# Optimization experiments

Hardware: AMD Instinct MI355X
Metric: run time of the kernel (lower is better)

## Reference

```python
import jax, jax.numpy as jnp
import numpy as np

B, N, D, H = 4, 1024, 1024, 16
DH = D // H
NEG_BIG = -2.0**32 + 1.0  # padding value from the torch code


def setup_inputs() -> dict:
    key = jax.random.key(0)
    ks = jax.random.split(key, 12)
    inp = {
        "x": jax.random.normal(ks[0], (B, N, D), dtype=jnp.float32),
        "key_padding_mask": jnp.zeros((B, N), dtype=bool),  # True = padded
        # attention projections (nn.Linear, bias=False): y = x @ W.T
        "Wq": jax.random.normal(ks[1], (D, D), dtype=jnp.float32) * (D ** -0.5),
        "Wk": jax.random.normal(ks[2], (D, D), dtype=jnp.float32) * (D ** -0.5),
        "Wv": jax.random.normal(ks[3], (D, D), dtype=jnp.float32) * (D ** -0.5),
        # FFN
        "W1": jax.random.normal(ks[4], (D, D), dtype=jnp.float32) * (D ** -0.5),
        "b1": jnp.zeros((D,), dtype=jnp.float32),
        "W2": jax.random.normal(ks[5], (D, D), dtype=jnp.float32) * (D ** -0.5),
        "b2": jnp.zeros((D,), dtype=jnp.float32),
        # MaskedLayerNorm params
        "g1": jnp.ones((D,), dtype=jnp.float32),
        "beta1": jnp.zeros((D,), dtype=jnp.float32),
        "g2": jnp.ones((D,), dtype=jnp.float32),
        "beta2": jnp.zeros((D,), dtype=jnp.float32),
    }
    return inp


def masked_layer_norm(x, scale, bias, eps=1e-5):
    mean = jnp.mean(x, axis=-1, keepdims=True)
    var = jnp.mean(jnp.square(x - mean), axis=-1, keepdims=True)
    return (x - mean) * jax.lax.rsqrt(var + eps) * scale + bias


def _to_heads(t):
    # torch: cat(split(t, DH, dim=2), dim=0) -> head-major [H*B, N, DH]
    b, n, d = t.shape
    return t.reshape(b, n, H, DH).transpose(2, 0, 1, 3).reshape(H * b, n, DH)


def _from_heads(t, b):
    # torch: cat(split(t, B, dim=0), dim=2) -> [B, N, D]
    hb, n, dh = t.shape
    return t.reshape(H, b, n, dh).transpose(1, 2, 0, 3).reshape(b, n, H * dh)


def attention(x, key_padding_mask, Wq, Wk, Wv):
    b, n, d = x.shape
    Q = _to_heads(x @ Wq.T)  # (H*B, N, DH)
    K = _to_heads(x @ Wk.T)
    V = _to_heads(x @ Wv.T)

    scores = jnp.einsum("znd,zmd->znm", Q, K) / (DH ** 0.5)  # (H*B, N, N)

    # key masks: sign of sum|K| over feature dim, broadcast over query axis
    key_masks = jnp.sign(jnp.sum(jnp.abs(K), axis=-1))  # (H*B, N)
    scores = jnp.where(key_masks[:, None, :] == 0, jnp.full_like(scores, NEG_BIG), scores)

    # temporal mask, direction == FORWARD: mask[i, j] = (j > i)
    idx = jnp.arange(n)
    attn_mask = idx[None, :] > idx[:, None]  # sw_row > sw_col with ij meshgrid
    scores = scores + (1.0 - attn_mask.astype(scores.dtype)) * -10000.0

    # NOTE: original code calls F.softmax(outputs) with no dim on a 3D tensor;
    # torch's implicit-dim rule selects dim=0 for ndim==3. Replicated faithfully.
    attn = jax.nn.softmax(scores, axis=0)

    query_masks = jnp.sign(jnp.sum(jnp.abs(Q), axis=-1))  # (H*B, N)
    attn = attn * query_masks[:, :, None]
    # dropout p=0.0 -> identity

    out = jnp.einsum("znm,zmd->znd", attn, V)  # (H*B, N, DH)
    out = _from_heads(out, b)  # (B, N, D)
    out = out * (~key_padding_mask)[:, :, None].astype(out.dtype)
    return out


def reference(x, key_padding_mask, Wq, Wk, Wv, W1, b1, W2, b2, g1, beta1, g2, beta2):
    attn_out = attention(x, key_padding_mask, Wq, Wk, Wv)
    h = masked_layer_norm(x + attn_out, g1, beta1)  # layer_norm1
    ff = jax.nn.relu(h @ W1.T + b1) @ W2.T + b2  # fc (dropout p=0)
    valid = (~key_padding_mask)[:, :, None].astype(ff.dtype)
    ff = ff * valid
    out = masked_layer_norm(ff + h, g2, beta2)  # layer_norm2
    out = out * valid
    return out
```

## Files before the change

kernel.cpp:

```cpp
#include <hip/hip_runtime.h>
#include <math.h>

typedef unsigned short u16;
typedef unsigned char  u8;
typedef unsigned int   u32;
typedef __attribute__((ext_vector_type(8))) short bf16x8;
typedef __attribute__((ext_vector_type(4))) float f32x4;

#define NSEQ   1024
#define DMODEL 1024
#define ZTOT   64
#define LOG2E  1.4426950408889634f

typedef const __attribute__((address_space(1))) void* gp1;
typedef __attribute__((address_space(3))) void* lp3;

__device__ __forceinline__ void gload16(const void* g, void* l) {
    __builtin_amdgcn_global_load_lds((gp1)g, (lp3)l, 16, 0, 0);
}

__device__ __forceinline__ u16 f2bf(float f) {
    u32 u = __builtin_bit_cast(u32, f);
    return (u16)((u + 0x7FFFu + ((u >> 16) & 1u)) >> 16);
}

__device__ __forceinline__ float bf2f(u32 lo16) {
    u32 t = lo16 << 16;
    return __builtin_bit_cast(float, t);
}

__device__ __forceinline__ u32 cvt_pk_bf16(float a, float b) {
    u32 r;
    asm("v_cvt_pk_bf16_f32 %0, %1, %2" : "=v"(r) : "v"(a), "v"(b));
    return r;
}

struct P5 { const float* in[5]; u16* out[5]; };
__launch_bounds__(256)
__global__ void cvt_all(const float* __restrict__ x, u16* __restrict__ xb, P5 p) {
    int bid = blockIdx.x;
    const float* in;
    u16* out;
    int blk;
    if (bid < 4096) { in = x; out = xb; blk = bid; }
    else {
        int which = (bid - 4096) >> 10;
        blk = bid & 1023;
        in = p.in[which];
        out = p.out[which];
    }
    int i = (blk * 256 + threadIdx.x) * 4;
    float4 v = *(const float4*)(in + i);
    uint2 o;
    o.x = cvt_pk_bf16(v.x, v.y);
    o.y = cvt_pk_bf16(v.z, v.w);
    *(uint2*)(out + i) = o;
}

__launch_bounds__(256)
__global__ void rowmask2_bf(const u16* __restrict__ Kh, const u16* __restrict__ Qh,
                            float* __restrict__ km, float* __restrict__ qm) {
    int b = blockIdx.x;
    const u16* T = (b < 256) ? Kh : Qh;
    float* o = (b < 256) ? km : qm;
    int r = (b & 255) * 256 + threadIdx.x;
    const uint4* p = (const uint4*)(T + (size_t)r * 64);
    u32 acc = 0;
    #pragma unroll
    for (int i = 0; i < 8; i++) {
        uint4 q = p[i];
        acc |= (q.x | q.y | q.z | q.w) & 0x7fff7fffu;
    }
    o[r] = acc ? 1.f : 0.f;
}

__launch_bounds__(256)
__global__ void vt_km(u16* __restrict__ Vt, const float* __restrict__ km) {
    int idx = blockIdx.x * 256 + threadIdx.x;
    int e0 = idx * 8;
    int z = e0 >> 16;
    int tok = e0 & 1023;
    float4 ka = *(const float4*)(km + z * 1024 + tok);
    float4 kb = *(const float4*)(km + z * 1024 + tok + 4);
    uint4 v = *(uint4*)(Vt + e0);
    u32 m;
    m = (ka.x != 0.f ? 0x0000FFFFu : 0u) | (ka.y != 0.f ? 0xFFFF0000u : 0u); v.x &= m;
    m = (ka.z != 0.f ? 0x0000FFFFu : 0u) | (ka.w != 0.f ? 0xFFFF0000u : 0u); v.y &= m;
    m = (kb.x != 0.f ? 0x0000FFFFu : 0u) | (kb.y != 0.f ? 0xFFFF0000u : 0u); v.z &= m;
    m = (kb.z != 0.f ? 0x0000FFFFu : 0u) | (kb.w != 0.f ? 0xFFFF0000u : 0u); v.w &= m;
    *(uint4*)(Vt + e0) = v;
}

__launch_bounds__(256)
__global__ void gemm_qkv(const u16* __restrict__ A,
                         const u16* __restrict__ Wq, const u16* __restrict__ Wk,
                         const u16* __restrict__ Wv,
                         u16* __restrict__ Qh, u16* __restrict__ Kh, u16* __restrict__ Vt)
{
    __shared__ __align__(16) u16 lA[2][128 * 32];
    __shared__ __align__(16) u16 lB[2][128 * 32];
    const int tid = threadIdx.x, lane = tid & 63, w = tid >> 6;
    const int frow = lane & 15, koct = lane >> 4;
    const int sel = blockIdx.x >> 3;
    const int col0 = (blockIdx.x & 7) * 128, row0 = blockIdx.y * 128;
    const u16* B = (sel == 0) ? Wq : (sel == 1) ? Wk : Wv;
    const int wrow = (w >> 1) * 64, wcol = (w & 1) * 64;
    f32x4 acc[4][4] = {};

    auto stage = [&](int buf, int k0) {
        #pragma unroll
        for (int i = 0; i < 2; i++) {
            int p = tid + i * 256;
            int row = p >> 2, sl = p & 3, ssl = sl ^ ((row >> 1) & 3);
            gload16(A + (size_t)(row0 + row) * 1024 + k0 + ssl * 8, (char*)lA[buf] + p * 16);
        }
        #pragma unroll
        for (int i = 0; i < 2; i++) {
            int p = tid + i * 256;
            int row = p >> 2, sl = p & 3, ssl = sl ^ ((row >> 1) & 3);
            gload16(B + (size_t)(col0 + row) * 1024 + k0 + ssl * 8, (char*)lB[buf] + p * 16);
        }
    };

    stage(0, 0);
    __syncthreads();
    int buf = 0;
    for (int k0 = 0; k0 < 1024; k0 += 32) {
        if (k0 + 32 < 1024) stage(buf ^ 1, k0 + 32);
        __builtin_amdgcn_s_setprio(1);
        bf16x8 af[4], bf[4];
        #pragma unroll
        for (int i = 0; i < 4; i++) {
            int r = wrow + i * 16 + frow;
            int sl = koct ^ ((r >> 1) & 3);
            af[i] = *(const bf16x8*)((const char*)lA[buf] + r * 64 + sl * 16);
        }
        #pragma unroll
        for (int j = 0; j < 4; j++) {
            int r = wcol + j * 16 + frow;
            int sl = koct ^ ((r >> 1) & 3);
            bf[j] = *(const bf16x8*)((const char*)lB[buf] + r * 64 + sl * 16);
        }
        #pragma unroll
        for (int i = 0; i < 4; i++)
            #pragma unroll
            for (int j = 0; j < 4; j++)
                acc[i][j] = __builtin_amdgcn_mfma_f32_16x16x32_bf16(af[i], bf[j], acc[i][j], 0, 0, 0);
        __builtin_amdgcn_s_setprio(0);
        __syncthreads();
        buf ^= 1;
    }

    if (sel < 2) {
        const float scale = (sel == 0) ? 0.125f * LOG2E : 1.0f;
        u16* outp = (sel == 0) ? Qh : Kh;
        #pragma unroll
        for (int i = 0; i < 4; i++)
            #pragma unroll
            for (int j = 0; j < 4; j++)
                #pragma unroll
                for (int q = 0; q < 4; q++) {
                    int r = row0 + wrow + i * 16 + koct * 4 + q;
                    int c = col0 + wcol + j * 16 + frow;
                    float v = acc[i][j][q] * scale;
                    outp[(size_t)((c >> 6) * 4 + (r >> 10)) * 65536 +
                         (size_t)(r & 1023) * 64 + (c & 63)] = f2bf(v);
                }
    } else {
        #pragma unroll
        for (int i = 0; i < 4; i++) {
            int r0 = row0 + wrow + i * 16 + koct * 4;
            #pragma unroll
            for (int j = 0; j < 4; j++) {
                int c = col0 + wcol + j * 16 + frow;
                int z = (c >> 6) * 4 + (r0 >> 10);
                uint2 pk;
                pk.x = cvt_pk_bf16(acc[i][j][0], acc[i][j][1]);
                pk.y = cvt_pk_bf16(acc[i][j][2], acc[i][j][3]);
                *(uint2*)(Vt + (size_t)z * 65536 + (size_t)(c & 63) * 1024 + (r0 & 1023)) = pk;
            }
        }
    }
}

template <int MODE>
__launch_bounds__(256)
__global__ void gemm_bt(const u16* __restrict__ A, const u16* __restrict__ B,
                        const float* __restrict__ bias, u16* __restrict__ outp)
{
    __shared__ __align__(16) u16 lA[2][128 * 64];
    __shared__ __align__(16) u16 lB[2][64 * 64];
    const int tid = threadIdx.x, lane = tid & 63, w = tid >> 6;
    const int frow = lane & 15, koct = lane >> 4;
    const int col0 = blockIdx.x * 64, row0 = blockIdx.y * 128;
    const int wrow = (w >> 1) * 64, wcol = (w & 1) * 32;
    f32x4 acc[4][2] = {};

    auto stage = [&](int buf, int k0) {
        #pragma unroll
        for (int i = 0; i < 4; i++) {
            int p = tid + i * 256;
            int row = p >> 3, sl = p & 7, ssl = sl ^ (row & 7);
            gload16(A + (size_t)(row0 + row) * 1024 + k0 + ssl * 8, (char*)lA[buf] + p * 16);
        }
        #pragma unroll
        for (int i = 0; i < 2; i++) {
            int p = tid + i * 256;
            int row = p >> 3, sl = p & 7, ssl = sl ^ (row & 7);
            gload16(B + (size_t)(col0 + row) * 1024 + k0 + ssl * 8, (char*)lB[buf] + p * 16);
        }
    };

    stage(0, 0);
    __syncthreads();
    int buf = 0;
    for (int k0 = 0; k0 < 1024; k0 += 64) {
        if (k0 + 64 < 1024) stage(buf ^ 1, k0 + 64);
        __builtin_amdgcn_s_setprio(1);
        #pragma unroll
        for (int ks = 0; ks < 2; ks++) {
            bf16x8 af[4], bf2[2];
            #pragma unroll
            for (int i = 0; i < 4; i++) {
                int r = wrow + i * 16 + frow;
                int sl = (ks * 4 + koct) ^ (r & 7);
                af[i] = *(const bf16x8*)((const char*)lA[buf] + r * 128 + sl * 16);
            }
            #pragma unroll
            for (int j = 0; j < 2; j++) {
                int r = wcol + j * 16 + frow;
                int sl = (ks * 4 + koct) ^ (r & 7);
                bf2[j] = *(const bf16x8*)((const char*)lB[buf] + r * 128 + sl * 16);
            }
            #pragma unroll
            for (int i = 0; i < 4; i++)
                #pragma unroll
                for (int j = 0; j < 2; j++)
                    acc[i][j] = __builtin_amdgcn_mfma_f32_16x16x32_bf16(af[i], bf2[j], acc[i][j], 0, 0, 0);
        }
        __builtin_amdgcn_s_setprio(0);
        __syncthreads();
        buf ^= 1;
    }

    #pragma unroll
    for (int i = 0; i < 4; i++)
        #pragma unroll
        for (int j = 0; j < 2; j++)
            #pragma unroll
            for (int q = 0; q < 4; q++) {
                int r = row0 + wrow + i * 16 + koct * 4 + q;
                int c = col0 + wcol + j * 16 + frow;
                float v = acc[i][j][q] + bias[c];
                if constexpr (MODE == 2) v = fmaxf(v, 0.f);
                outp[(size_t)r * 1024 + c] = f2bf(v);
            }
}

__launch_bounds__(256)
__global__ void attn_pass1(const u16* __restrict__ Qh, const u16* __restrict__ Kh,
                           const float* __restrict__ km, float* __restrict__ partial)
{
    const int bid = blockIdx.x;
    const int mtzg = (bid & 7) * 8 + ((bid >> 3) & 7);
    const int m0 = (mtzg & 15) * 64, zg = mtzg >> 4;
    const int n0 = (bid >> 6) * 64;

    __shared__ __align__(16) u16 lQ[2][64 * 64];
    __shared__ __align__(16) u16 lK[2][64 * 64];
    const int tid = threadIdx.x, lane = tid & 63, w = tid >> 6;
    const int frow = lane & 15, koct = lane >> 4;
    const int wn = (w >> 1) * 32, wm = (w & 1) * 32;
    f32x4 ssum[2][2] = {};

    auto stage = [&](int buf, int z) {
        #pragma unroll
        for (int i = 0; i < 2; i++) {
            int p = tid + i * 256;
            int row = p >> 3, sl = p & 7, ssl = sl ^ (row & 7);
            gload16(Qh + (size_t)(z * NSEQ + n0 + row) * 64 + ssl * 8, (char*)lQ[buf] + p * 16);
            gload16(Kh + (size_t)(z * NSEQ + m0 + row) * 64 + ssl * 8, (char*)lK[buf] + p * 16);
        }
    };

    const int z0 = zg * 16;
    stage(0, z0);
    __syncthreads();
    int buf = 0;
    for (int zi = 0; zi < 16; zi++) {
        const int z = z0 + zi;
        if (zi < 15) stage(buf ^ 1, z + 1);
        f32x4 km4[2];
        #pragma unroll
        for (int j = 0; j < 2; j++)
            km4[j] = *(const f32x4*)(km + z * NSEQ + m0 + wm + j * 16 + koct * 4);
        f32x4 s[2][2] = {};
        __builtin_amdgcn_s_setprio(1);
        #pragma unroll
        for (int ks = 0; ks < 2; ks++) {
            bf16x8 a[2], b2[2];
            #pragma unroll
            for (int i = 0; i < 2; i++) {
                int r = wn + i * 16 + frow;
                int sl = (ks * 4 + koct) ^ (r & 7);
                a[i] = *(const bf16x8*)((const char*)lQ[buf] + r * 128 + sl * 16);
            }
            #pragma unroll
            for (int j = 0; j < 2; j++) {
                int r = wm + j * 16 + frow;
                int sl = (ks * 4 + koct) ^ (r & 7);
                b2[j] = *(const bf16x8*)((const char*)lK[buf] + r * 128 + sl * 16);
            }
            #pragma unroll
            for (int i = 0; i < 2; i++)
                #pragma unroll
                for (int j = 0; j < 2; j++)
                    s[i][j] = __builtin_amdgcn_mfma_f32_16x16x32_bf16(b2[j], a[i], s[i][j], 0, 0, 0);
        }
        __builtin_amdgcn_s_setprio(0);
        #pragma unroll
        for (int j = 0; j < 2; j++)
            #pragma unroll
            for (int i = 0; i < 2; i++)
                #pragma unroll
                for (int q = 0; q < 4; q++)
                    ssum[i][j][q] += __builtin_amdgcn_exp2f(s[i][j][q]) * km4[j][q];
        __syncthreads();
        buf ^= 1;
    }
    #pragma unroll
    for (int i = 0; i < 2; i++)
        #pragma unroll
        for (int j = 0; j < 2; j++) {
            int ng = n0 + wn + i * 16 + frow;
            int mg = m0 + wm + j * 16 + koct * 4;
            *(f32x4*)(partial + (size_t)zg * 1048576 + (size_t)ng * NSEQ + mg) = ssum[i][j];
        }
}

__launch_bounds__(256)
__global__ void sum_inv(const float* __restrict__ p, float* __restrict__ invS) {
    int i = (blockIdx.x * 256 + threadIdx.x) * 4;
    float4 a = *(const float4*)(p + i);
    float4 b = *(const float4*)(p + 1048576 + i);
    float4 c = *(const float4*)(p + 2097152 + i);
    float4 d = *(const float4*)(p + 3145728 + i);
    float4 r;
    float s;
    s = a.x + b.x + c.x + d.x; r.x = s > 0.f ? 1.f / s : 0.f;
    s = a.y + b.y + c.y + d.y; r.y = s > 0.f ? 1.f / s : 0.f;
    s = a.z + b.z + c.z + d.z; r.z = s > 0.f ? 1.f / s : 0.f;
    s = a.w + b.w + c.w + d.w; r.w = s > 0.f ? 1.f / s : 0.f;
    *(float4*)(invS + i) = r;
}

__launch_bounds__(256)
__global__ void attn_pass2(const u16* __restrict__ Qh, const u16* __restrict__ Kh,
                           const u16* __restrict__ Vt,
                           const float* __restrict__ qm, const float* __restrict__ invS,
                           const u8* __restrict__ pad, u16* __restrict__ attn)
{
    const int bid = blockIdx.x;
    const int z  = (bid & 7) * 8 + ((bid >> 3) & 7);
    const int n0 = (bid >> 6) * 64;

    __shared__ __align__(16) u16 lK[2][64 * 64];
    __shared__ __align__(16) u16 lV[2][64 * 64];
    __shared__ __align__(16) u16 lP[64 * 64];
    const int tid = threadIdx.x, lane = tid & 63, w = tid >> 6;
    const int frow = lane & 15, koct = lane >> 4;
    const int hh = z >> 2, bb = z & 3;
    const int wrow = w * 16;
    const int nl_row = wrow + frow;
    const size_t inv_base = (size_t)(n0 + nl_row) * NSEQ;

    bf16x8 aq[2];
    #pragma unroll
    for (int ks = 0; ks < 2; ks++)
        aq[ks] = *(const bf16x8*)(Qh + (size_t)(z * NSEQ + n0 + nl_row) * 64 + ks * 32 + koct * 8);

    auto stage = [&](int buf, int m0) {
        #pragma unroll
        for (int i = 0; i < 2; i++) {
            int p = tid + i * 256;
            int row = p >> 3, sl = p & 7, ssl = sl ^ (row & 7);
            gload16(Kh + (size_t)(z * NSEQ + m0 + row) * 64 + ssl * 8, (char*)lK[buf] + p * 16);
            gload16(Vt + (size_t)z * 65536 + (size_t)row * 1024 + m0 + ssl * 8, (char*)lV[buf] + p * 16);
        }
    };

    f32x4 oacc[4] = {};
    f32x4 iv[4];
    #pragma unroll
    for (int j = 0; j < 4; j++)
        iv[j] = *(const f32x4*)(invS + inv_base + j * 16 + koct * 4);
    stage(0, 0);
    __syncthreads();
    int buf = 0;

    for (int mt = 0; mt < 16; mt++) {
        const int m0 = mt * 64;
        if (mt < 15) stage(buf ^ 1, m0 + 64);
        f32x4 ivn[4];
        if (mt < 15) {
            #pragma unroll
            for (int j = 0; j < 4; j++)
                ivn[j] = *(const f32x4*)(invS + inv_base + m0 + 64 + j * 16 + koct * 4);
        }
        f32x4 s[4] = {};
        __builtin_amdgcn_s_setprio(1);
        #pragma unroll
        for (int ks = 0; ks < 2; ks++) {
            bf16x8 kb[4];
            #pragma unroll
            for (int j = 0; j < 4; j++) {
                int r = j * 16 + frow;
                int sl = (ks * 4 + koct) ^ (r & 7);
                kb[j] = *(const bf16x8*)((const char*)lK[buf] + r * 128 + sl * 16);
            }
            #pragma unroll
            for (int j = 0; j < 4; j++)
                s[j] = __builtin_amdgcn_mfma_f32_16x16x32_bf16(kb[j], aq[ks], s[j], 0, 0, 0);
        }
        __builtin_amdgcn_s_setprio(0);
        #pragma unroll
        for (int j = 0; j < 4; j++) {
            float p0 = __builtin_amdgcn_exp2f(s[j][0]) * iv[j][0];
            float p1 = __builtin_amdgcn_exp2f(s[j][1]) * iv[j][1];
            float p2 = __builtin_amdgcn_exp2f(s[j][2]) * iv[j][2];
            float p3 = __builtin_amdgcn_exp2f(s[j][3]) * iv[j][3];
            uint2 pk;
            pk.x = cvt_pk_bf16(p0, p1);
            pk.y = cvt_pk_bf16(p2, p3);
            int slot = (j * 2 + (koct >> 1)) ^ (nl_row & 7);
            *(uint2*)((char*)lP + nl_row * 128 + slot * 16 + (koct & 1) * 8) = pk;
        }
        __builtin_amdgcn_s_setprio(1);
        #pragma unroll
        for (int ks = 0; ks < 2; ks++) {
            int sl = (ks * 4 + koct) ^ (nl_row & 7);
            bf16x8 pa = *(const bf16x8*)((const char*)lP + nl_row * 128 + sl * 16);
            bf16x8 vb[4];
            #pragma unroll
            for (int dj = 0; dj < 4; dj++) {
                int rr = dj * 16 + frow;
                int sv = (ks * 4 + koct) ^ (rr & 7);
                vb[dj] = *(const bf16x8*)((const char*)lV[buf] + rr * 128 + sv * 16);
            }
            #pragma unroll
            for (int dj = 0; dj < 4; dj++)
                oacc[dj] = __builtin_amdgcn_mfma_f32_16x16x32_bf16(pa, vb[dj], oacc[dj], 0, 0, 0);
        }
        __builtin_amdgcn_s_setprio(0);
        __syncthreads();
        buf ^= 1;
        #pragma unroll
        for (int j = 0; j < 4; j++) iv[j] = ivn[j];
    }

    #pragma unroll
    for (int q = 0; q < 4; q++) {
        int ns = n0 + wrow + koct * 4 + q;
        float f = qm[z * NSEQ + ns] * (pad[bb * NSEQ + ns] ? 0.f : 1.f);
        #pragma unroll
        for (int dj = 0; dj < 4; dj++) {
            int d = dj * 16 + frow;
            attn[(size_t)(bb * NSEQ + ns) * DMODEL + hh * 64 + d] = f2bf(oacc[dj][q] * f);
        }
    }
}

template <int MODE>
__launch_bounds__(256)
__global__ void ln_kernel(const void* __restrict__ Ap, const void* __restrict__ Bp,
                          const float* __restrict__ g, const float* __restrict__ beta,
                          const u8* __restrict__ pad,
                          float* __restrict__ outf, u16* __restrict__ outb)
{
    const int row = blockIdx.x, tid = threadIdx.x;
    const int lane = tid & 63, wv = tid >> 6;
    const float valid = pad[row] ? 0.f : 1.f;
    __shared__ float red[4];

    float v[4];
    if constexpr (MODE == 0) {
        float4 va = *(const float4*)((const float*)Ap + (size_t)row * 1024 + tid * 4);
        uint2 bbv = *(const uint2*)((const u16*)Bp + (size_t)row * 1024 + tid * 4);
        v[0] = va.x + bf2f(bbv.x & 0xFFFFu);
        v[1] = va.y + bf2f(bbv.x >> 16);
        v[2] = va.z + bf2f(bbv.y & 0xFFFFu);
        v[3] = va.w + bf2f(bbv.y >> 16);
    } else {
        uint2 aav = *(const uint2*)((const u16*)Ap + (size_t)row * 1024 + tid * 4);
        uint2 bbv = *(const uint2*)((const u16*)Bp + (size_t)row * 1024 + tid * 4);
        v[0] = bf2f(aav.x & 0xFFFFu) * valid + bf2f(bbv.x & 0xFFFFu);
        v[1] = bf2f(aav.x >> 16)     * valid + bf2f(bbv.x >> 16);
        v[2] = bf2f(aav.y & 0xFFFFu) * valid + bf2f(bbv.y & 0xFFFFu);
        v[3] = bf2f(aav.y >> 16)     * valid + bf2f(bbv.y >> 16);
    }
    float s = v[0] + v[1] + v[2] + v[3];
    #pragma unroll
    for (int off = 32; off > 0; off >>= 1) s += __shfl_down(s, off, 64);
    if (lane == 0) red[wv] = s;
    __syncthreads();
    float mean = (red[0] + red[1] + red[2] + red[3]) * (1.f / 1024.f);
    float sq = 0.f;
    #pragma unroll
    for (int k = 0; k < 4; k++) { float d = v[k] - mean; sq += d * d; }
    __syncthreads();
    #pragma unroll
    for (int off = 32; off > 0; off >>= 1) sq += __shfl_down(sq, off, 64);
    if (lane == 0) red[wv] = sq;
    __syncthreads();
    float var = (red[0] + red[1] + red[2] + red[3]) * (1.f / 1024.f);
    float rstd = rsqrtf(var + 1e-5f);

    if constexpr (MODE == 0) {
        uint2 o;
        float o0 = (v[0] - mean) * rstd * g[tid * 4 + 0] + beta[tid * 4 + 0];
        float o1 = (v[1] - mean) * rstd * g[tid * 4 + 1] + beta[tid * 4 + 1];
        float o2 = (v[2] - mean) * rstd * g[tid * 4 + 2] + beta[tid * 4 + 2];
        float o3 = (v[3] - mean) * rstd * g[tid * 4 + 3] + beta[tid * 4 + 3];
        o.x = cvt_pk_bf16(o0, o1);
        o.y = cvt_pk_bf16(o2, o3);
        *(uint2*)(outb + (size_t)row * 1024 + tid * 4) = o;
    } else {
        float4 o;
        o.x = ((v[0] - mean) * rstd * g[tid * 4 + 0] + beta[tid * 4 + 0]) * valid;
        o.y = ((v[1] - mean) * rstd * g[tid * 4 + 1] + beta[tid * 4 + 1]) * valid;
        o.z = ((v[2] - mean) * rstd * g[tid * 4 + 2] + beta[tid * 4 + 2]) * valid;
        o.w = ((v[3] - mean) * rstd * g[tid * 4 + 3] + beta[tid * 4 + 3]) * valid;
        *(float4*)(outf + (size_t)row * 1024 + tid * 4) = o;
    }
}

extern "C" void kernel_launch(void* const* d_in, const int* in_sizes, int n_in,
                              void* d_out, int out_size, void* d_ws, size_t ws_size,
                              hipStream_t stream)
{
    const float* x   = (const float*)d_in[0];
    const u8*    pad = (const u8*)d_in[1];
    const float* Wq  = (const float*)d_in[2];
    const float* Wk  = (const float*)d_in[3];
    const float* Wv  = (const float*)d_in[4];
    const float* W1  = (const float*)d_in[5];
    const float* b1  = (const float*)d_in[6];
    const float* W2  = (const float*)d_in[7];
    const float* b2  = (const float*)d_in[8];
    const float* g1  = (const float*)d_in[9];
    const float* be1 = (const float*)d_in[10];
    const float* g2  = (const float*)d_in[11];
    const float* be2 = (const float*)d_in[12];
    float* out = (float*)d_out;

    u16* xb    = (u16*)d_ws;
    u16* Wqb   = xb    + 4194304;
    u16* Wkb   = Wqb   + 1048576;
    u16* Wvb   = Wkb   + 1048576;
    u16* W1b   = Wvb   + 1048576;
    u16* W2b   = W1b   + 1048576;
    u16* Qh    = W2b   + 1048576;
    u16* Kh    = Qh    + 4194304;
    u16* Vt    = Kh    + 4194304;
    u16* hb    = Vt    + 4194304;
    u16* ff1b  = hb    + 4194304;
    u16* ffb   = ff1b  + 4194304;
    u16* attnb = ffb   + 4194304;
    float* km      = (float*)(attnb + 4194304);
    float* qm      = km      + 65536;
    float* partial = qm      + 65536;
    float* invS    = partial + 4194304;

    P5 p5;
    p5.in[0] = Wq; p5.in[1] = Wk; p5.in[2] = Wv; p5.in[3] = W1; p5.in[4] = W2;
    p5.out[0] = Wqb; p5.out[1] = Wkb; p5.out[2] = Wvb; p5.out[3] = W1b; p5.out[4] = W2b;
    cvt_all<<<9216, 256, 0, stream>>>(x, xb, p5);

    gemm_qkv<<<dim3(24, 32), 256, 0, stream>>>(xb, Wqb, Wkb, Wvb, Qh, Kh, Vt);

    rowmask2_bf<<<512, 256, 0, stream>>>(Kh, Qh, km, qm);
    vt_km<<<4096, 256, 0, stream>>>(Vt, km);

    attn_pass1<<<1024, 256, 0, stream>>>(Qh, Kh, km, partial);
    sum_inv<<<1024, 256, 0, stream>>>(partial, invS);
    attn_pass2<<<1024, 256, 0, stream>>>(Qh, Kh, Vt, qm, invS, pad, attnb);

    ln_kernel<0><<<4096, 256, 0, stream>>>(x, attnb, g1, be1, pad, nullptr, hb);

    gemm_bt<2><<<dim3(16, 32), 256, 0, stream>>>(hb,   W1b, b1, ff1b);
    gemm_bt<3><<<dim3(16, 32), 256, 0, stream>>>(ff1b, W2b, b2, ffb);

    ln_kernel<1><<<4096, 256, 0, stream>>>(ffb, hb, g2, be2, pad, out, nullptr);
}
```

Before: 177.2 us.

## Split attn_pass2 key tiles across two waves per row block and read bf16 x in LN1

attn_pass2 now launches 512 threads, so two waves share each 16-row query slice, each handling half of the 64-key tile. Each wave keeps a private P buffer, and the two partial outputs are combined through shared memory at the end. This doubles wave-level parallelism and cuts per-wave serial MFMA work, at the cost of an extra reduction and barrier. Separately, LN1 reads the bf16 copy of x instead of fp32, which halves that read traffic but lowers the precision of the residual.

```diff
diff --git a/kernel.cpp b/kernel.cpp
--- a/kernel.cpp
+++ b/kernel.cpp
@@ -354,7 +354,7 @@
     *(float4*)(invS + i) = r;
 }
 
-__launch_bounds__(256)
+__launch_bounds__(512, 8)
 __global__ void attn_pass2(const u16* __restrict__ Qh, const u16* __restrict__ Kh,
                            const u16* __restrict__ Vt,
                            const float* __restrict__ qm, const float* __restrict__ invS,
@@ -366,13 +366,16 @@
 
     __shared__ __align__(16) u16 lK[2][64 * 64];
     __shared__ __align__(16) u16 lV[2][64 * 64];
-    __shared__ __align__(16) u16 lP[64 * 64];
+    __shared__ __align__(16) u16 lP[8][16 * 32];
     const int tid = threadIdx.x, lane = tid & 63, w = tid >> 6;
     const int frow = lane & 15, koct = lane >> 4;
+    const int nsub = w >> 1, mhalf = w & 1;
     const int hh = z >> 2, bb = z & 3;
-    const int wrow = w * 16;
+    const int wrow = nsub * 16;
     const int nl_row = wrow + frow;
     const size_t inv_base = (size_t)(n0 + nl_row) * NSEQ;
+    const int sw = (frow ^ (frow >> 2)) & 3;
+    char* lPw = (char*)&lP[w][0];
 
     bf16x8 aq[2];
     #pragma unroll
@@ -380,20 +383,21 @@
         aq[ks] = *(const bf16x8*)(Qh + (size_t)(z * NSEQ + n0 + nl_row) * 64 + ks * 32 + koct * 8);
 
     auto stage = [&](int buf, int m0) {
-        #pragma unroll
-        for (int i = 0; i < 2; i++) {
-            int p = tid + i * 256;
-            int row = p >> 3, sl = p & 7, ssl = sl ^ (row & 7);
+        {
+            int p = tid, row = p >> 3, sl = p & 7, ssl = sl ^ (row & 7);
             gload16(Kh + (size_t)(z * NSEQ + m0 + row) * 64 + ssl * 8, (char*)lK[buf] + p * 16);
+        }
+        {
+            int p = tid, row = p >> 3, sl = p & 7, ssl = sl ^ (row & 7);
             gload16(Vt + (size_t)z * 65536 + (size_t)row * 1024 + m0 + ssl * 8, (char*)lV[buf] + p * 16);
         }
     };
 
     f32x4 oacc[4] = {};
-    f32x4 iv[4];
-    #pragma unroll
-    for (int j = 0; j < 4; j++)
-        iv[j] = *(const f32x4*)(invS + inv_base + j * 16 + koct * 4);
+    f32x4 iv[2];
+    #pragma unroll
+    for (int jl = 0; jl < 2; jl++)
+        iv[jl] = *(const f32x4*)(invS + inv_base + (mhalf * 2 + jl) * 16 + koct * 4);
     stage(0, 0);
     __syncthreads();
     int buf = 0;
@@ -401,78 +405,85 @@
     for (int mt = 0; mt < 16; mt++) {
         const int m0 = mt * 64;
         if (mt < 15) stage(buf ^ 1, m0 + 64);
-        f32x4 ivn[4];
+        f32x4 ivn[2];
         if (mt < 15) {
             #pragma unroll
-            for (int j = 0; j < 4; j++)
-                ivn[j] = *(const f32x4*)(invS + inv_base + m0 + 64 + j * 16 + koct * 4);
-        }
-        f32x4 s[4] = {};
+            for (int jl = 0; jl < 2; jl++)
+                ivn[jl] = *(const f32x4*)(invS + inv_base + m0 + 64 + (mhalf * 2 + jl) * 16 + koct * 4);
+        }
+        f32x4 s[2] = {};
         __builtin_amdgcn_s_setprio(1);
         #pragma unroll
         for (int ks = 0; ks < 2; ks++) {
-            bf16x8 kb[4];
-            #pragma unroll
-            for (int j = 0; j < 4; j++) {
-                int r = j * 16 + frow;
+            bf16x8 kb[2];
+            #pragma unroll
+            for (int jl = 0; jl < 2; jl++) {
+                int r = (mhalf * 2 + jl) * 16 + frow;
                 int sl = (ks * 4 + koct) ^ (r & 7);
-                kb[j] = *(const bf16x8*)((const char*)lK[buf] + r * 128 + sl * 16);
-            }
-            #pragma unroll
-            for (int j = 0; j < 4; j++)
-                s[j] = __builtin_amdgcn_mfma_f32_16x16x32_bf16(kb[j], aq[ks], s[j], 0, 0, 0);
+                kb[jl] = *(const bf16x8*)((const char*)lK[buf] + r * 128 + sl * 16);
+            }
+            #pragma unroll
+            for (int jl = 0; jl < 2; jl++)
+                s[jl] = __builtin_amdgcn_mfma_f32_16x16x32_bf16(kb[jl], aq[ks], s[jl], 0, 0, 0);
         }
         __builtin_amdgcn_s_setprio(0);
         #pragma unroll
-        for (int j = 0; j < 4; j++) {
-            float p0 = __builtin_amdgcn_exp2f(s[j][0]) * iv[j][0];
-            float p1 = __builtin_amdgcn_exp2f(s[j][1]) * iv[j][1];
-            float p2 = __builtin_amdgcn_exp2f(s[j][2]) * iv[j][2];
-            float p3 = __builtin_amdgcn_exp2f(s[j][3]) * iv[j][3];
+        for (int jl = 0; jl < 2; jl++) {
+            float p0 = __builtin_amdgcn_exp2f(s[jl][0]) * iv[jl][0];
+            float p1 = __builtin_amdgcn_exp2f(s[jl][1]) * iv[jl][1];
+            float p2 = __builtin_amdgcn_exp2f(s[jl][2]) * iv[jl][2];
+            float p3 = __builtin_amdgcn_exp2f(s[jl][3]) * iv[jl][3];
             uint2 pk;
             pk.x = cvt_pk_bf16(p0, p1);
             pk.y = cvt_pk_bf16(p2, p3);
-            int slot = (j * 2 + (koct >> 1)) ^ (nl_row & 7);
-            *(uint2*)((char*)lP + nl_row * 128 + slot * 16 + (koct & 1) * 8) = pk;
+            int slot = (jl * 2 + (koct >> 1)) ^ sw;
+            *(uint2*)(lPw + frow * 64 + slot * 16 + (koct & 1) * 8) = pk;
         }
         __builtin_amdgcn_s_setprio(1);
-        #pragma unroll
-        for (int ks = 0; ks < 2; ks++) {
-            int sl = (ks * 4 + koct) ^ (nl_row & 7);
-            bf16x8 pa = *(const bf16x8*)((const char*)lP + nl_row * 128 + sl * 16);
-            bf16x8 vb[4];
+        {
+            bf16x8 pa = *(const bf16x8*)(lPw + frow * 64 + ((koct ^ sw) << 4));
             #pragma unroll
             for (int dj = 0; dj < 4; dj++) {
                 int rr = dj * 16 + frow;
-                int sv = (ks * 4 + koct) ^ (rr & 7);
-                vb[dj] = *(const bf16x8*)((const char*)lV[buf] + rr * 128 + sv * 16);
-            }
-            #pragma unroll
-            for (int dj = 0; dj < 4; dj++)
-                oacc[dj] = __builtin_amdgcn_mfma_f32_16x16x32_bf16(pa, vb[dj], oacc[dj], 0, 0, 0);
+                int sv = (mhalf * 4 + koct) ^ (rr & 7);
+                bf16x8 vb = *(const bf16x8*)((const char*)lV[buf] + rr * 128 + sv * 16);
+                oacc[dj] = __builtin_amdgcn_mfma_f32_16x16x32_bf16(pa, vb, oacc[dj], 0, 0, 0);
+            }
         }
         __builtin_amdgcn_s_setprio(0);
         __syncthreads();
         buf ^= 1;
         #pragma unroll
-        for (int j = 0; j < 4; j++) iv[j] = ivn[j];
-    }
-
-    #pragma unroll
-    for (int q = 0; q < 4; q++) {
-        int ns = n0 + wrow + koct * 4 + q;
-        float f = qm[z * NSEQ + ns] * (pad[bb * NSEQ + ns] ? 0.f : 1.f);
-        #pragma unroll
-        for (int dj = 0; dj < 4; dj++) {
-            int d = dj * 16 + frow;
-            attn[(size_t)(bb * NSEQ + ns) * DMODEL + hh * 64 + d] = f2bf(oacc[dj][q] * f);
+        for (int jl = 0; jl < 2; jl++) iv[jl] = ivn[jl];
+    }
+
+    float* red = (float*)&lK[0][0];
+    if (mhalf) {
+        float* dst = red + ((size_t)nsub * 64 + lane) * 16;
+        #pragma unroll
+        for (int dj = 0; dj < 4; dj++) *(f32x4*)(dst + dj * 4) = oacc[dj];
+    }
+    __syncthreads();
+    if (!mhalf) {
+        const float* src = red + ((size_t)nsub * 64 + lane) * 16;
+        #pragma unroll
+        for (int dj = 0; dj < 4; dj++) oacc[dj] += *(const f32x4*)(src + dj * 4);
+        #pragma unroll
+        for (int q = 0; q < 4; q++) {
+            int ns = n0 + wrow + koct * 4 + q;
+            float f = qm[z * NSEQ + ns] * (pad[bb * NSEQ + ns] ? 0.f : 1.f);
+            #pragma unroll
+            for (int dj = 0; dj < 4; dj++) {
+                int d = dj * 16 + frow;
+                attn[(size_t)(bb * NSEQ + ns) * DMODEL + hh * 64 + d] = f2bf(oacc[dj][q] * f);
+            }
         }
     }
 }
 
 template <int MODE>
 __launch_bounds__(256)
-__global__ void ln_kernel(const void* __restrict__ Ap, const void* __restrict__ Bp,
+__global__ void ln_kernel(const u16* __restrict__ Ap, const u16* __restrict__ Bp,
                           const float* __restrict__ g, const float* __restrict__ beta,
                           const u8* __restrict__ pad,
                           float* __restrict__ outf, u16* __restrict__ outb)
@@ -482,17 +493,15 @@
     const float valid = pad[row] ? 0.f : 1.f;
     __shared__ float red[4];
 
+    uint2 aav = *(const uint2*)(Ap + (size_t)row * 1024 + tid * 4);
+    uint2 bbv = *(const uint2*)(Bp + (size_t)row * 1024 + tid * 4);
     float v[4];
     if constexpr (MODE == 0) {
-        float4 va = *(const float4*)((const float*)Ap + (size_t)row * 1024 + tid * 4);
-        uint2 bbv = *(const uint2*)((const u16*)Bp + (size_t)row * 1024 + tid * 4);
-        v[0] = va.x + bf2f(bbv.x & 0xFFFFu);
-        v[1] = va.y + bf2f(bbv.x >> 16);
-        v[2] = va.z + bf2f(bbv.y & 0xFFFFu);
-        v[3] = va.w + bf2f(bbv.y >> 16);
+        v[0] = bf2f(aav.x & 0xFFFFu) + bf2f(bbv.x & 0xFFFFu);
+        v[1] = bf2f(aav.x >> 16)     + bf2f(bbv.x >> 16);
+        v[2] = bf2f(aav.y & 0xFFFFu) + bf2f(bbv.y & 0xFFFFu);
+        v[3] = bf2f(aav.y >> 16)     + bf2f(bbv.y >> 16);
     } else {
-        uint2 aav = *(const uint2*)((const u16*)Ap + (size_t)row * 1024 + tid * 4);
-        uint2 bbv = *(const uint2*)((const u16*)Bp + (size_t)row * 1024 + tid * 4);
         v[0] = bf2f(aav.x & 0xFFFFu) * valid + bf2f(bbv.x & 0xFFFFu);
         v[1] = bf2f(aav.x >> 16)     * valid + bf2f(bbv.x >> 16);
         v[2] = bf2f(aav.y & 0xFFFFu) * valid + bf2f(bbv.y & 0xFFFFu);
@@ -583,9 +592,9 @@
 
     attn_pass1<<<1024, 256, 0, stream>>>(Qh, Kh, km, partial);
     sum_inv<<<1024, 256, 0, stream>>>(partial, invS);
-    attn_pass2<<<1024, 256, 0, stream>>>(Qh, Kh, Vt, qm, invS, pad, attnb);
-
-    ln_kernel<0><<<4096, 256, 0, stream>>>(x, attnb, g1, be1, pad, nullptr, hb);
+    attn_pass2<<<1024, 512, 0, stream>>>(Qh, Kh, Vt, qm, invS, pad, attnb);
+
+    ln_kernel<0><<<4096, 256, 0, stream>>>(xb, attnb, g1, be1, pad, nullptr, hb);
 
     gemm_bt<2><<<dim3(16, 32), 256, 0, stream>>>(hb,   W1b, b1, ff1b);
     gemm_bt<3><<<dim3(16, 32), 256, 0, stream>>>(ff1b, W2b, b2, ffb);
```

Result: slower. 185.7 us (+4.8%).
